# Performance work log

Measured on AMD Instinct MI355X. Metric: run time of the kernel, lower is better.

Reference implementation:

```python
import jax, jax.numpy as jnp
import numpy as np

EMB = 256
D_INNER = 512                         # expand=2 * d_model
HEADDIM = 64
NHEADS = D_INNER // HEADDIM           # 8
DSTATE = 128
DCONV = 4
CONV_DIM = D_INNER + 2 * DSTATE       # 768 (ngroups=1)
D_IN_PROJ = 2 * D_INNER + 2 * DSTATE + NHEADS  # 1288
LN_EPS = 1e-5


def _layernorm(x, w, b):
    m = jnp.mean(x, axis=-1, keepdims=True)
    v = jnp.mean((x - m) ** 2, axis=-1, keepdims=True)
    return (x - m) * jax.lax.rsqrt(v + LN_EPS) * w + b


def _wn_linear(x, g, v, b):
    # torch weight_norm(dim=0): w = g * v / ||v|| per output row
    w = g[:, None] * v / jnp.linalg.norm(v, axis=1, keepdims=True)
    return x @ w.T + b


def _ssm_scan(x, dt, A, Bm, Cm):
    # x: (b,l,h,p)  dt: (b,l,h)  A: (h,)  Bm/Cm: (b,l,n)
    dA = jnp.exp(dt * A)           # (b,l,h), A<0 so dA in (0,1)
    dtx = dt[..., None] * x        # (b,l,h,p)
    bsz = x.shape[0]

    def step(h, inp):
        dA_t, dtx_t, B_t, C_t = inp
        h = h * dA_t[:, :, None, None] + dtx_t[..., None] * B_t[:, None, None, :]
        y = jnp.einsum('bhpn,bn->bhp', h, C_t)
        return h, y

    h0 = jnp.zeros((bsz, NHEADS, HEADDIM, DSTATE), x.dtype)
    xs = (jnp.swapaxes(dA, 0, 1), jnp.swapaxes(dtx, 0, 1),
          jnp.swapaxes(Bm, 0, 1), jnp.swapaxes(Cm, 0, 1))
    _, ys = jax.lax.scan(step, h0, xs)
    return jnp.swapaxes(ys, 0, 1)  # (b,l,h,p)


def _mamba2(u, in_proj_w, conv_w, conv_b, dt_bias, A_log, D_param, ssm_norm_w, out_proj_w):
    B, L, _ = u.shape
    zxbcdt = u @ in_proj_w.T                       # (B,L,1288)
    z_gate = zxbcdt[..., :D_INNER]
    xBC = zxbcdt[..., D_INNER:D_INNER + CONV_DIM]
    dt = zxbcdt[..., D_INNER + CONV_DIM:]
    # causal depthwise conv1d
    xp = jnp.pad(xBC, ((0, 0), (DCONV - 1, 0), (0, 0)))
    xc = jax.lax.conv_general_dilated(
        jnp.swapaxes(xp, 1, 2), conv_w[:, None, :], (1,), 'VALID',
        feature_group_count=CONV_DIM, dimension_numbers=('NCH', 'OIH', 'NCH'))
    xc = jax.nn.silu(jnp.swapaxes(xc, 1, 2) + conv_b)
    x = xc[..., :D_INNER].reshape(B, L, NHEADS, HEADDIM)
    Bm = xc[..., D_INNER:D_INNER + DSTATE]
    Cm = xc[..., D_INNER + DSTATE:]
    dt = jax.nn.softplus(dt + dt_bias)             # (B,L,H)
    A = -jnp.exp(A_log)                            # (H,)
    y = _ssm_scan(x, dt, A, Bm, Cm) + D_param[None, None, :, None] * x
    y = y.reshape(B, L, D_INNER)
    # gated RMSNorm (norm_before_gate=False): rmsnorm(y * silu(z)) * w
    yg = y * jax.nn.silu(z_gate)
    yn = yg * jax.lax.rsqrt(jnp.mean(yg ** 2, axis=-1, keepdims=True) + LN_EPS) * ssm_norm_w
    return yn @ out_proj_w.T


def setup_inputs() -> dict:
    key = jax.random.key(0)
    ks = jax.random.split(key, 12)
    B, NU, NA = 1, 64, 512

    def rn(k, shape, scale):
        return jax.random.normal(k, shape, dtype=jnp.float32) * scale

    z = rn(ks[0], (B, NU, NA, EMB), 1.0)
    in_proj_w = rn(ks[1], (D_IN_PROJ, EMB), EMB ** -0.5)
    conv_w = rn(ks[2], (CONV_DIM, DCONV), DCONV ** -0.5)
    conv_b = rn(ks[3], (CONV_DIM,), 0.02)
    dt_bias = jnp.log(jnp.expm1(jax.random.uniform(ks[4], (NHEADS,), minval=0.001, maxval=0.1)))
    A_log = jnp.log(jax.random.uniform(ks[5], (NHEADS,), minval=1.0, maxval=16.0))
    D_param = jnp.ones((NHEADS,), dtype=jnp.float32)
    ssm_norm_w = jnp.ones((D_INNER,), dtype=jnp.float32)
    out_proj_w = rn(ks[6], (EMB, D_INNER), D_INNER ** -0.5)
    ff_v = rn(ks[7], (EMB, EMB), EMB ** -0.5)
    ff_g = jnp.linalg.norm(ff_v, axis=1)
    ff_b = jnp.zeros((EMB,), dtype=jnp.float32)
    fc1_v = rn(ks[8], (EMB, EMB), EMB ** -0.5)
    fc1_g = jnp.linalg.norm(fc1_v, axis=1)
    fc1_b = jnp.zeros((EMB,), dtype=jnp.float32)
    fc2_v = rn(ks[9], (EMB, EMB), EMB ** -0.5)
    fc2_g = jnp.linalg.norm(fc2_v, axis=1)
    fc2_b = jnp.zeros((EMB,), dtype=jnp.float32)
    return {
        'z': z,
        'ln1_w': jnp.ones((EMB,), dtype=jnp.float32), 'ln1_b': jnp.zeros((EMB,), dtype=jnp.float32),
        'in_proj_w': in_proj_w, 'conv_w': conv_w, 'conv_b': conv_b,
        'dt_bias': dt_bias, 'A_log': A_log, 'D_param': D_param,
        'ssm_norm_w': ssm_norm_w, 'out_proj_w': out_proj_w,
        'ff_g': ff_g, 'ff_v': ff_v, 'ff_b': ff_b,
        'ln2_w': jnp.ones((EMB,), dtype=jnp.float32), 'ln2_b': jnp.zeros((EMB,), dtype=jnp.float32),
        'fc1_g': fc1_g, 'fc1_v': fc1_v, 'fc1_b': fc1_b,
        'fc2_g': fc2_g, 'fc2_v': fc2_v, 'fc2_b': fc2_b,
    }


def reference(z, ln1_w, ln1_b, in_proj_w, conv_w, conv_b, dt_bias, A_log, D_param,
              ssm_norm_w, out_proj_w, ff_g, ff_v, ff_b, ln2_w, ln2_b,
              fc1_g, fc1_v, fc1_b, fc2_g, fc2_v, fc2_b):
    b, nu, na, e = z.shape
    # MambaBlock: z + ff(mamba(norm(z)))
    u = _layernorm(z, ln1_w, ln1_b).reshape(-1, na, e)
    y = _mamba2(u, in_proj_w, conv_w, conv_b, dt_bias, A_log, D_param, ssm_norm_w, out_proj_w)
    y = _wn_linear(y, ff_g, ff_v, ff_b).reshape(b, nu, na, e)
    z = z + y
    # NormFF: z + Lin2(GELU(Lin1(LN(z))))  (dropout inactive in eval)
    h = _layernorm(z, ln2_w, ln2_b)
    h = jax.nn.gelu(_wn_linear(h, fc1_g, fc1_v, fc1_b), approximate=False)
    h = _wn_linear(h, fc2_g, fc2_v, fc2_b)
    return z + h
```

## Files before the change

### kernel.cpp

```cpp
#include <hip/hip_runtime.h>
#include <stdint.h>
#include <math.h>

#define EMB       256
#define D_INNER   512
#define HEADDIM   64
#define NHEADS    8
#define DSTATE    128
#define DCONV     4
#define CONV_DIM  768
#define LN_EPS    1e-5f
#define NBATCH    64
#define SEQLEN    512
#define NTOK      (NBATCH*SEQLEN)

typedef __attribute__((ext_vector_type(8))) short          short8;
typedef __attribute__((ext_vector_type(8))) unsigned short u16x8;
typedef __attribute__((ext_vector_type(4))) unsigned short u16x4;
typedef __attribute__((ext_vector_type(4))) float          f32x4;

__device__ __forceinline__ float bfb(unsigned short u) {
    union { unsigned int i; float f; } x; x.i = ((unsigned int)u) << 16; return x.f;
}
__device__ __forceinline__ unsigned short fbf(float f) {
    union { float f; unsigned int i; } x; x.f = f;
    unsigned int i = x.i;
    unsigned int lsb = (i >> 16) & 1u;
    i += 0x7fffu + lsb;
    return (unsigned short)(i >> 16);
}

__device__ __forceinline__ void gld16(const unsigned short* g, unsigned short* l) {
    __builtin_amdgcn_global_load_lds((const __attribute__((address_space(1))) void*)g,
                                     (__attribute__((address_space(3))) void*)l, 16, 0, 0);
}

__global__ __launch_bounds__(256) void cvt2_k(const float* __restrict__ a, unsigned short* __restrict__ oa, int na,
                                              const float* __restrict__ b, unsigned short* __restrict__ ob, int nb) {
    int i = blockIdx.x * 256 + threadIdx.x;
    if (i < na) oa[i] = fbf(a[i]);
    else { i -= na; if (i < nb) ob[i] = fbf(b[i]); }
}

__global__ __launch_bounds__(256) void wnorm3_k(const float* __restrict__ g0, const float* __restrict__ v0, unsigned short* __restrict__ o0,
                                                const float* __restrict__ g1, const float* __restrict__ v1, unsigned short* __restrict__ o1,
                                                const float* __restrict__ g2, const float* __restrict__ v2, unsigned short* __restrict__ o2) {
    int o = blockIdx.x & 255, s = blockIdx.x >> 8, tid = threadIdx.x;
    const float* g = s == 0 ? g0 : (s == 1 ? g1 : g2);
    const float* v = s == 0 ? v0 : (s == 1 ? v1 : v2);
    unsigned short* wout = s == 0 ? o0 : (s == 1 ? o1 : o2);
    float x = v[(size_t)o * 256 + tid];
    float q = x * x;
    __shared__ float sm[4];
    #pragma unroll
    for (int d = 32; d; d >>= 1) q += __shfl_down(q, d);
    if ((tid & 63) == 0) sm[tid >> 6] = q;
    __syncthreads();
    float tot = sm[0] + sm[1] + sm[2] + sm[3];
    float scale = g[o] * rsqrtf(tot);
    wout[(size_t)o * 256 + tid] = fbf(x * scale);
}

__global__ __launch_bounds__(256) void wco_k(const unsigned short* __restrict__ wff,
                                             const unsigned short* __restrict__ outWb,
                                             unsigned short* __restrict__ wco) {
    int i = blockIdx.x, tid = threadIdx.x;
    __shared__ float row[256];
    row[tid] = bfb(wff[(size_t)i * 256 + tid]);
    __syncthreads();
    #pragma unroll
    for (int half = 0; half < 2; half++) {
        int k = tid + half * 256;
        float acc = 0.f;
        for (int j = 0; j < 256; j++)
            acc += row[j] * bfb(outWb[(size_t)j * 512 + k]);
        wco[(size_t)i * 512 + k] = fbf(acc);
    }
}

__global__ __launch_bounds__(256) void ln_k(const float* __restrict__ in,
                                            const float* __restrict__ w,
                                            const float* __restrict__ b,
                                            unsigned short* __restrict__ out) {
    int tok = blockIdx.x, tid = threadIdx.x;
    size_t idx = (size_t)tok * 256 + tid;
    float x = in[idx];
    __shared__ float sm[8];
    float s = x;
    #pragma unroll
    for (int o = 32; o; o >>= 1) s += __shfl_down(s, o);
    if ((tid & 63) == 0) sm[tid >> 6] = s;
    __syncthreads();
    float mean = (sm[0] + sm[1] + sm[2] + sm[3]) * (1.f / 256.f);
    float d = x - mean;
    float q = d * d;
    #pragma unroll
    for (int o = 32; o; o >>= 1) q += __shfl_down(q, o);
    if ((tid & 63) == 0) sm[4 + (tid >> 6)] = q;
    __syncthreads();
    float var = (sm[4] + sm[5] + sm[6] + sm[7]) * (1.f / 256.f);
    out[idx] = fbf(d * rsqrtf(var + LN_EPS) * w[tid] + b[tid]);
}

#define BMT 128
#define BNT 128
#define BKT 32
template<int EPI, int NBN>
__global__ __launch_bounds__(256, 2) void gemm_k(const unsigned short* __restrict__ A,
                                                 const unsigned short* __restrict__ Bw,
                                                 int K, int N,
                                                 unsigned short* __restrict__ out_b,
                                                 float* __restrict__ out_f,
                                                 const float* __restrict__ bias,
                                                 const float* __restrict__ res_f,
                                                 unsigned short* __restrict__ out2_b) {
    __shared__ __align__(16) unsigned short smem[16384];
    int tid = threadIdx.x;
    int d = blockIdx.x;
    const int cpx = (256 * NBN) >> 3;
    int logical = (d & 7) * cpx + (d >> 3);
    int bm = logical / NBN;
    int bn = logical % NBN;
    int lane = tid & 63, w = tid >> 6;
    int wr = w >> 1, wc = w & 1;
    int fr = lane & 15, fq = lane >> 4;

    int rsub = w * 16 + (lane >> 2);
    int cl   = ((lane & 3) ^ ((rsub >> 1) & 3)) << 3;
    const unsigned short* gA0 = A  + (size_t)(bm * BMT + rsub)      * K + cl;
    const unsigned short* gA1 = A  + (size_t)(bm * BMT + rsub + 64) * K + cl;
    const unsigned short* gB0 = Bw + (size_t)(bn * BNT + rsub)      * K + cl;
    const unsigned short* gB1 = Bw + (size_t)(bn * BNT + rsub + 64) * K + cl;

    f32x4 acc[4][4];
    #pragma unroll
    for (int m = 0; m < 4; m++)
        #pragma unroll
        for (int n = 0; n < 4; n++)
            #pragma unroll
            for (int r = 0; r < 4; r++) acc[m][n][r] = 0.f;

    auto AS = [&](int buf) { return &smem[buf * 4096]; };
    auto BS = [&](int buf) { return &smem[8192 + buf * 4096]; };
    auto STAGE = [&](int buf, int k0) {
        gld16(gA0 + k0, AS(buf) + w * 512);
        gld16(gA1 + k0, AS(buf) + 2048 + w * 512);
        gld16(gB0 + k0, BS(buf) + w * 512);
        gld16(gB1 + k0, BS(buf) + 2048 + w * 512);
    };

    int nt = K / BKT;
    STAGE(0, 0);
    STAGE(1, BKT);
    for (int t = 0; t < nt; ++t) {
        int buf = t & 1;
        if (t < nt - 1) asm volatile("s_waitcnt vmcnt(4)" ::: "memory");
        else            asm volatile("s_waitcnt vmcnt(0)" ::: "memory");
        __builtin_amdgcn_s_barrier();
        short8 af[4], bf_[4];
        #pragma unroll
        for (int m = 0; m < 4; m++) {
            int ra = wr * 64 + m * 16 + fr;
            af[m] = *(const short8*)&AS(buf)[ra * 32 + ((fq ^ ((ra >> 1) & 3)) << 3)];
        }
        #pragma unroll
        for (int n = 0; n < 4; n++) {
            int rb = wc * 64 + n * 16 + fr;
            bf_[n] = *(const short8*)&BS(buf)[rb * 32 + ((fq ^ ((rb >> 1) & 3)) << 3)];
        }
        asm volatile("s_waitcnt lgkmcnt(0)" ::: "memory");
        __builtin_amdgcn_sched_barrier(0);
        __builtin_amdgcn_s_barrier();
        if (t + 2 < nt) STAGE(buf, (t + 2) * BKT);
        __builtin_amdgcn_s_setprio(1);
        #pragma unroll
        for (int m = 0; m < 4; m++)
            #pragma unroll
            for (int n = 0; n < 4; n++)
                acc[m][n] = __builtin_amdgcn_mfma_f32_16x16x32_bf16(af[m], bf_[n], acc[m][n], 0, 0, 0);
        __builtin_amdgcn_s_setprio(0);
    }
    __builtin_amdgcn_s_barrier();

    if (EPI == 1 && bn == 10) {
        #pragma unroll
        for (int m = 0; m < 4; m++)
            #pragma unroll
            for (int n = 0; n < 4; n++)
                #pragma unroll
                for (int r = 0; r < 4; r++) {
                    int grow = bm * BMT + wr * 64 + m * 16 + fq * 4 + r;
                    int gcol = 1280 + wc * 64 + n * 16 + fr;
                    if (gcol < 1288) {
                        float a2 = acc[m][n][r] + bias[gcol - 1280];
                        out_f[(size_t)grow * 8 + (gcol - 1280)] =
                            a2 > 20.f ? a2 : log1pf(expf(a2));
                    }
                }
    } else if (EPI == 0 || EPI == 1) {
        unsigned short* cb = smem;
        #pragma unroll
        for (int s = 0; s < 2; s++) {
            if (wr == s) {
                #pragma unroll
                for (int m = 0; m < 4; m++)
                    #pragma unroll
                    for (int n = 0; n < 4; n++)
                        #pragma unroll
                        for (int r = 0; r < 4; r++)
                            cb[(m * 16 + fq * 4 + r) * 136 + wc * 64 + n * 16 + fr] =
                                fbf(acc[m][n][r]);
            }
            __syncthreads();
            #pragma unroll
            for (int k = 0; k < 4; k++) {
                int g = k * 256 + tid;
                int row = g >> 4, col = (g & 15) << 3;
                u16x8 v = *(const u16x8*)&cb[row * 136 + col];
                int grow = bm * BMT + s * 64 + row;
                int gc = bn * BNT + col;
                if (EPI == 0) {
                    *(u16x8*)&out_b[(size_t)grow * N + gc] = v;
                } else {
                    if (gc < 512) *(u16x8*)&out_b[(size_t)grow * 512 + gc] = v;
                    else          *(u16x8*)&out2_b[(size_t)grow * 768 + (gc - 512)] = v;
                }
            }
            __syncthreads();
        }
    } else {
        float* fb = (float*)smem;
        #pragma unroll
        for (int s = 0; s < 4; s++) {
            if (wr == (s >> 1)) {
                int mp = s & 1;
                #pragma unroll
                for (int mm = 0; mm < 2; mm++)
                    #pragma unroll
                    for (int n = 0; n < 4; n++)
                        #pragma unroll
                        for (int r = 0; r < 4; r++)
                            fb[(mm * 16 + fq * 4 + r) * 132 + wc * 64 + n * 16 + fr] =
                                acc[mp * 2 + mm][n][r];
            }
            __syncthreads();
            #pragma unroll
            for (int k = 0; k < 4; k++) {
                int g = k * 256 + tid;
                int row = g >> 5, col = (g & 31) << 2;
                f32x4 v = *(const f32x4*)&fb[row * 132 + col];
                int grow = bm * BMT + (s >> 1) * 64 + (s & 1) * 32 + row;
                int gc = bn * BNT + col;
                size_t idx = (size_t)grow * 256 + gc;
                if (EPI == 2) {
                    f32x4 rr = *(const f32x4*)&res_f[idx];
                    f32x4 o;
                    #pragma unroll
                    for (int j = 0; j < 4; j++) o[j] = rr[j] + v[j] + bias[gc + j];
                    *(f32x4*)&out_f[idx] = o;
                } else {
                    u16x4 o;
                    #pragma unroll
                    for (int j = 0; j < 4; j++) {
                        float x = v[j] + bias[gc + j];
                        o[j] = fbf(0.5f * x * (1.f + erff(x * 0.70710678118654752f)));
                    }
                    *(u16x4*)&out_b[idx] = o;
                }
            }
            __syncthreads();
        }
    }
}

__global__ __launch_bounds__(256) void halo_k(const unsigned short* __restrict__ xbc,
                                              unsigned short* __restrict__ halo) {
    int blk = blockIdx.x;
    int b = blk / 3, c = blk % 3 + 1;
    int tid = threadIdx.x;
    for (int i = tid; i < 288; i += 256) {
        int j = i / 96, off = (i % 96) * 8;
        size_t tok = (size_t)b * 512 + c * 128 - 3 + j;
        *(u16x8*)&halo[((size_t)(b * 4 + c) * 3 + j) * 768 + off] =
            *(const u16x8*)&xbc[tok * 768 + off];
    }
}

__global__ __launch_bounds__(256) void conv_k(unsigned short* xbc,
                                              const unsigned short* __restrict__ halo,
                                              const float* __restrict__ cw,
                                              const float* __restrict__ cb) {
    int b  = blockIdx.y;
    int c  = blockIdx.z;
    int c0 = blockIdx.x * 64;
    int t0 = c * 128;
    int tid = threadIdx.x;
    int cth = tid & 63;
    int rq  = tid >> 6;
    __shared__ unsigned short sraw[131][72];

    int ca = c0 + cth;
    float w0 = cw[ca * 4 + 0], w1 = cw[ca * 4 + 1];
    float w2 = cw[ca * 4 + 2], w3 = cw[ca * 4 + 3];
    float bias = cb[ca];

    if (tid < 192) {
        int j = tid >> 6, cc = tid & 63;
        sraw[j][cc] = (c == 0) ? (unsigned short)0
            : halo[((size_t)(b * 4 + c) * 3 + j) * 768 + c0 + cc];
    }
    for (int idx = tid; idx < 1024; idx += 256) {
        int lt = idx >> 3, cg = idx & 7;
        *(u16x8*)&sraw[3 + lt][cg * 8] =
            *(const u16x8*)&xbc[((size_t)(b * 512 + t0 + lt)) * 768 + c0 + cg * 8];
    }
    __syncthreads();
    #pragma unroll 4
    for (int i = 0; i < 32; i++) {
        int lt = rq + 4 * i;
        float acc = bias
            + bfb(sraw[lt + 0][cth]) * w0
            + bfb(sraw[lt + 1][cth]) * w1
            + bfb(sraw[lt + 2][cth]) * w2
            + bfb(sraw[lt + 3][cth]) * w3;
        acc = acc / (1.f + expf(-acc));
        xbc[((size_t)(b * 512 + t0 + lt)) * 768 + c0 + cth] = fbf(acc);
    }
}

#define CPAD 136
#define TPAD 56
#define TOFF(r) ((((r) >> 4) & 3) << 3)
__global__ __launch_bounds__(256) void ssd_k(const unsigned short* __restrict__ xc,
                                             const float* __restrict__ dts,
                                             const float* __restrict__ A_log,
                                             const float* __restrict__ D_param,
                                             unsigned short* __restrict__ y) {
    __shared__ unsigned short Ct[32][CPAD];
    __shared__ unsigned short Bt[32][CPAD];
    __shared__ unsigned short BtT[128][TPAD];
    __shared__ unsigned short DXT[64][TPAD];
    __shared__ unsigned short LG[32][40];
    __shared__ unsigned short hB[64][CPAD];
    __shared__ unsigned short Yb[32][72];
    __shared__ float scum[32], sdt2[32], sEC[32];
    __shared__ float sET[32][36];

    int d = blockIdx.x;
    int b = (d & 7) | (((d >> 6) & 7) << 3);
    int h = (d >> 3) & 7;
    int tid = threadIdx.x;
    int w = tid >> 6;
    int lane = tid & 63;
    int fr = lane & 15, fq = lane >> 4;

    float A_h = -expf(A_log[h]);
    float D_h = D_param[h];

    f32x4 hacc[8];
    #pragma unroll
    for (int nf = 0; nf < 8; nf++)
        #pragma unroll
        for (int r = 0; r < 4; r++) hacc[nf][r] = 0.f;

    int t  = tid >> 3;
    int e8 = tid & 7;

    u16x8 bv0, bv1, cv0, cv1, xv;
    {
        const unsigned short* row = &xc[((size_t)b * 512 + t) * 768];
        bv0 = *(const u16x8*)&row[512 + e8 * 16];
        bv1 = *(const u16x8*)&row[512 + e8 * 16 + 8];
        cv0 = *(const u16x8*)&row[640 + e8 * 16];
        cv1 = *(const u16x8*)&row[640 + e8 * 16 + 8];
        xv  = *(const u16x8*)&row[h * 64 + e8 * 8];
    }

    for (int c = 0; c < 16; ++c) {
        size_t tok0 = (size_t)b * 512 + c * 32;
        *(u16x8*)&Ct[t][e8 * 16]     = cv0;
        *(u16x8*)&Ct[t][e8 * 16 + 8] = cv1;
        *(u16x8*)&Bt[t][e8 * 16]     = bv0;
        *(u16x8*)&Bt[t][e8 * 16 + 8] = bv1;
        if (tid < 32) {
            float dtv = dts[(tok0 + tid) * 8 + h];
            sdt2[tid] = dtv;
            float la = dtv * A_h;
            #pragma unroll
            for (int dd = 1; dd < 32; dd <<= 1) {
                float up = __shfl_up(la, dd);
                if (lane >= dd) la += up;
            }
            scum[tid] = la;
        }
        __syncthreads();
        float cumQ = scum[31];
        if (tid < 32) sEC[tid] = expf(scum[tid]);
        {
            float dtv = sdt2[t];
            float wgt = expf(cumQ - scum[t]);
            int tof = TOFF(e8 * 16);
            #pragma unroll
            for (int j = 0; j < 8; j++) {
                float dtx = dtv * bfb(xv[j]);
                int rr = e8 * 8 + j;
                DXT[rr][t + TOFF(rr)] = fbf(dtx);
                BtT[e8 * 16 + j][t + tof]     = fbf(wgt * bfb(bv0[j]));
                BtT[e8 * 16 + 8 + j][t + tof] = fbf(wgt * bfb(bv1[j]));
            }
        }
        #pragma unroll
        for (int k = 0; k < 4; k++) {
            int idx = tid * 4 + k;
            int tt = idx >> 5, tq = idx & 31;
            sET[tt][tq] = (tq <= tt) ? expf(scum[tt] - scum[tq]) : 0.f;
        }
        #pragma unroll
        for (int nf = 0; nf < 8; nf++)
            #pragma unroll
            for (int r = 0; r < 4; r++)
                hB[w * 16 + fq * 4 + r][nf * 16 + fr] = fbf(hacc[nf][r]);
        u16x8 nbv0, nbv1, ncv0, ncv1, nxv;
        {
            size_t ptok = (c + 1 < 16) ? (tok0 + 32 + t) : (tok0 + t);
            const unsigned short* row = &xc[ptok * 768];
            nbv0 = *(const u16x8*)&row[512 + e8 * 16];
            nbv1 = *(const u16x8*)&row[512 + e8 * 16 + 8];
            ncv0 = *(const u16x8*)&row[640 + e8 * 16];
            ncv1 = *(const u16x8*)&row[640 + e8 * 16 + 8];
            nxv  = *(const u16x8*)&row[h * 64 + e8 * 8];
        }
        __syncthreads();
        {
            int m = w >> 1, nf = w & 1;
            f32x4 g;
            #pragma unroll
            for (int r = 0; r < 4; r++) g[r] = 0.f;
            #pragma unroll
            for (int ks = 0; ks < 4; ks++) {
                short8 ca = *(const short8*)&Ct[m * 16 + fr][ks * 32 + fq * 8];
                short8 bb = *(const short8*)&Bt[nf * 16 + fr][ks * 32 + fq * 8];
                g = __builtin_amdgcn_mfma_f32_16x16x32_bf16(ca, bb, g, 0, 0, 0);
            }
            #pragma unroll
            for (int r = 0; r < 4; r++) {
                int tt = m * 16 + fq * 4 + r;
                int tq = nf * 16 + fr;
                LG[tt][tq] = fbf(g[r] * sET[tt][tq]);
            }
        }
        __syncthreads();
        f32x4 Yi[2];
        #pragma unroll
        for (int m = 0; m < 2; m++)
            #pragma unroll
            for (int r = 0; r < 4; r++) Yi[m][r] = 0.f;
        #pragma unroll
        for (int ks = 0; ks < 4; ks++) {
            short8 a0 = *(const short8*)&Ct[fr][ks * 32 + fq * 8];
            short8 a1 = *(const short8*)&Ct[16 + fr][ks * 32 + fq * 8];
            short8 hb = *(const short8*)&hB[w * 16 + fr][ks * 32 + fq * 8];
            Yi[0] = __builtin_amdgcn_mfma_f32_16x16x32_bf16(a0, hb, Yi[0], 0, 0, 0);
            Yi[1] = __builtin_amdgcn_mfma_f32_16x16x32_bf16(a1, hb, Yi[1], 0, 0, 0);
        }
        #pragma unroll
        for (int m = 0; m < 2; m++)
            #pragma unroll
            for (int r = 0; r < 4; r++) Yi[m][r] *= sEC[m * 16 + fq * 4 + r];
        {
            int wof = TOFF(w * 16);
            short8 a0 = *(const short8*)&LG[fr][fq * 8];
            short8 a1 = *(const short8*)&LG[16 + fr][fq * 8];
            short8 dx = *(const short8*)&DXT[w * 16 + fr][fq * 8 + wof];
            Yi[0] = __builtin_amdgcn_mfma_f32_16x16x32_bf16(a0, dx, Yi[0], 0, 0, 0);
            Yi[1] = __builtin_amdgcn_mfma_f32_16x16x32_bf16(a1, dx, Yi[1], 0, 0, 0);
        }
        {
            float ecq = sEC[31];
            #pragma unroll
            for (int nf = 0; nf < 8; nf++)
                #pragma unroll
                for (int r = 0; r < 4; r++) hacc[nf][r] *= ecq;
            int wof = TOFF(w * 16);
            short8 ax = *(const short8*)&DXT[w * 16 + fr][fq * 8 + wof];
            #pragma unroll
            for (int nf = 0; nf < 8; nf++) {
                short8 bb = *(const short8*)&BtT[nf * 16 + fr][fq * 8 + TOFF(nf * 16)];
                hacc[nf] = __builtin_amdgcn_mfma_f32_16x16x32_bf16(ax, bb, hacc[nf], 0, 0, 0);
            }
        }
        #pragma unroll
        for (int m = 0; m < 2; m++)
            #pragma unroll
            for (int r = 0; r < 4; r++) {
                int tt = m * 16 + fq * 4 + r;
                Yb[tt][w * 16 + fr] = fbf(Yi[m][r]);
            }
        __syncthreads();
        {
            u16x8 yv = *(const u16x8*)&Yb[t][e8 * 8];
            u16x8 ov;
            #pragma unroll
            for (int j = 0; j < 8; j++)
                ov[j] = fbf(bfb(yv[j]) + D_h * bfb(xv[j]));
            *(u16x8*)&y[(tok0 + t) * 512 + h * 64 + e8 * 8] = ov;
        }
        bv0 = nbv0; bv1 = nbv1; cv0 = ncv0; cv1 = ncv1; xv = nxv;
    }
}

__global__ __launch_bounds__(256) void gate_k(const unsigned short* __restrict__ y,
                                              const unsigned short* __restrict__ zg,
                                              const float* __restrict__ nw,
                                              unsigned short* __restrict__ yn) {
    int tok = blockIdx.x, tid = threadIdx.x;
    size_t base = (size_t)tok * 512;
    float gv[2];
    float q = 0.f;
    #pragma unroll
    for (int j = 0; j < 2; j++) {
        int c = tid + j * 256;
        float yy = bfb(y[base + c]);
        float zz = bfb(zg[base + c]);
        float s = zz / (1.f + expf(-zz));
        float t = yy * s;
        gv[j] = t;
        q += t * t;
    }
    __shared__ float sm[4];
    #pragma unroll
    for (int o = 32; o; o >>= 1) q += __shfl_down(q, o);
    if ((tid & 63) == 0) sm[tid >> 6] = q;
    __syncthreads();
    float ms = (sm[0] + sm[1] + sm[2] + sm[3]) * (1.f / 512.f);
    float r = rsqrtf(ms + LN_EPS);
    #pragma unroll
    for (int j = 0; j < 2; j++) {
        int c = tid + j * 256;
        yn[base + c] = fbf(gv[j] * r * nw[c]);
    }
}

extern "C" void kernel_launch(void* const* d_in, const int* in_sizes, int n_in,
                              void* d_out, int out_size, void* d_ws, size_t ws_size,
                              hipStream_t stream) {
    if (n_in < 22) return;
    static const int setup_sizes[22] = {8388608,256,256,329728,3072,768,8,8,8,512,
                                        131072,256,65536,256,256,256,256,65536,256,256,65536,256};
    for (int i = 0; i < 22; i++) if (in_sizes[i] != setup_sizes[i]) return;

    const float* z      = (const float*)d_in[0];
    const float* ln1w   = (const float*)d_in[1];
    const float* ln1b   = (const float*)d_in[2];
    const float* inW    = (const float*)d_in[3];
    const float* convw  = (const float*)d_in[4];
    const float* convb  = (const float*)d_in[5];
    const float* dtb    = (const float*)d_in[6];
    const float* Alog   = (const float*)d_in[7];
    const float* Dp     = (const float*)d_in[8];
    const float* normw  = (const float*)d_in[9];
    const float* outW   = (const float*)d_in[10];
    const float* ffg    = (const float*)d_in[11];
    const float* ffv    = (const float*)d_in[12];
    const float* ffb    = (const float*)d_in[13];
    const float* ln2w   = (const float*)d_in[14];
    const float* ln2b   = (const float*)d_in[15];
    const float* fc1g   = (const float*)d_in[16];
    const float* fc1v   = (const float*)d_in[17];
    const float* fc1b   = (const float*)d_in[18];
    const float* fc2g   = (const float*)d_in[19];
    const float* fc2v   = (const float*)d_in[20];
    const float* fc2b   = (const float*)d_in[21];
    float* out = (float*)d_out;
    (void)out_size;

    char* ws = (char*)d_ws;
    const size_t SLOT_A = (size_t)NTOK * 768 * 2;
    const size_t SLOT_B = (size_t)NTOK * 512 * 2;
    const size_t SLOT_C = (size_t)NTOK * 512 * 2;
    const size_t SLOT_D = (size_t)NTOK * 256 * 2;
    const size_t SLOT_E = (size_t)NTOK * 8 * 4;
    const size_t SLOT_W = (size_t)256 * 256 * 2;
    const size_t SLOT_WI = (size_t)1288 * 256 * 2;
    const size_t SLOT_WO = (size_t)256 * 512 * 2;
    const size_t SLOT_WC = (size_t)256 * 512 * 2;
    const size_t SLOT_H  = (size_t)256 * 3 * 768 * 2;
    char* pA = ws;
    char* pB = pA + SLOT_A;
    char* pC = pB + SLOT_B;
    char* pD = pC + SLOT_C;
    char* pE = pD + SLOT_D;
    char* pW = pE + SLOT_E;
    char* pWI = pW + 3 * SLOT_W;
    char* pWO = pWI + SLOT_WI;
    char* pWC = pWO + SLOT_WO;
    char* pH  = pWC + SLOT_WC;
    size_t need = SLOT_A + SLOT_B + SLOT_C + SLOT_D + SLOT_E + 3 * SLOT_W + SLOT_WI + SLOT_WO + SLOT_WC + SLOT_H;
    if (ws_size < need) return;

    unsigned short* xbc = (unsigned short*)pA;
    unsigned short* yn  = (unsigned short*)pA;
    unsigned short* t2  = (unsigned short*)(pA + (size_t)NTOK * 512 * 2);
    unsigned short* y   = (unsigned short*)pB;
    float*          z2  = (float*)pB;
    unsigned short* zgb = (unsigned short*)pC;
    unsigned short* u   = (unsigned short*)pD;
    unsigned short* h1  = (unsigned short*)pD;
    float*          dts = (float*)pE;
    unsigned short* wff  = (unsigned short*)pW;
    unsigned short* wfc1 = (unsigned short*)(pW + SLOT_W);
    unsigned short* wfc2 = (unsigned short*)(pW + 2 * SLOT_W);
    unsigned short* inWb = (unsigned short*)pWI;
    unsigned short* outWb = (unsigned short*)pWO;
    unsigned short* wco  = (unsigned short*)pWC;
    unsigned short* halo = (unsigned short*)pH;

    cvt2_k<<<(1288 * 256 + 131072 + 255) / 256, 256, 0, stream>>>(inW, inWb, 1288 * 256,
                                                                  outW, outWb, 131072);
    wnorm3_k<<<768, 256, 0, stream>>>(ffg, ffv, wff, fc1g, fc1v, wfc1, fc2g, fc2v, wfc2);
    wco_k<<<256, 256, 0, stream>>>(wff, outWb, wco);
    ln_k<<<NTOK, 256, 0, stream>>>(z, ln1w, ln1b, u);
    gemm_k<1, 11><<<256 * 11, 256, 0, stream>>>(u, inWb, 256, 1288,
                                                zgb, dts, dtb, nullptr, xbc);
    halo_k<<<192, 256, 0, stream>>>(xbc, halo);
    conv_k<<<dim3(12, 64, 4), 256, 0, stream>>>(xbc, halo, convw, convb);
    ssd_k<<<NBATCH * NHEADS, 256, 0, stream>>>(xbc, dts, Alog, Dp, y);
    gate_k<<<NTOK, 256, 0, stream>>>(y, zgb, normw, yn);
    gemm_k<2, 2><<<256 * 2, 256, 0, stream>>>(yn, wco, 512, 256,
                                              nullptr, z2, ffb, z, nullptr);
    ln_k<<<NTOK, 256, 0, stream>>>(z2, ln2w, ln2b, t2);
    gemm_k<3, 2><<<256 * 2, 256, 0, stream>>>(t2, wfc1, 256, 256,
                                              h1, nullptr, fc1b, nullptr, nullptr);
    gemm_k<2, 2><<<256 * 2, 256, 0, stream>>>(h1, wfc2, 256, 256,
                                              nullptr, out, fc2b, z2, nullptr);
}
```

Before: 290.2 us.

## Split SSD scan over state dimension halves to double block count

Adds an ssd2_k kernel that splits the 128-wide state dimension into two halves of 64, launching 1024 blocks instead of 512 so more of the GPU is occupied during the sequential chunk scan. Each half writes a partial output to a separate buffer, and gate_k sums the two partials before gating. The extra buffer is used only when the workspace is large enough, otherwise the old path runs. The cost is redundant recomputation of the intra-chunk terms and dt cumsums in both halves, an extra 32 MB output write and read, and partial sums rounded to bf16 before they are added.

```diff
diff --git a/kernel.cpp b/kernel.cpp
--- a/kernel.cpp
+++ b/kernel.cpp
@@ -331,6 +331,7 @@
 #define CPAD 136
 #define TPAD 56
 #define TOFF(r) ((((r) >> 4) & 3) << 3)
+
 __global__ __launch_bounds__(256) void ssd_k(const unsigned short* __restrict__ xc,
                                              const float* __restrict__ dts,
                                              const float* __restrict__ A_log,
@@ -509,7 +510,187 @@
     }
 }
 
+#define CPAD2 72
+__global__ __launch_bounds__(256) void ssd2_k(const unsigned short* __restrict__ xc,
+                                              const float* __restrict__ dts,
+                                              const float* __restrict__ A_log,
+                                              const float* __restrict__ D_param,
+                                              unsigned short* __restrict__ y0,
+                                              unsigned short* __restrict__ y1) {
+    __shared__ unsigned short Ct[32][CPAD2];
+    __shared__ unsigned short Bt[32][CPAD2];
+    __shared__ unsigned short BtT[64][TPAD];
+    __shared__ unsigned short DXT[64][TPAD];
+    __shared__ unsigned short LG[32][40];
+    __shared__ unsigned short hB[64][CPAD2];
+    __shared__ unsigned short Yb[32][72];
+    __shared__ float scum[32], sdt2[32], sEC[32];
+    __shared__ float sET[32][36];
+
+    int d = blockIdx.x;
+    int b  = (d & 7) | (((d >> 7) & 7) << 3);
+    int h  = (d >> 3) & 7;
+    int ph = (d >> 6) & 1;
+    int n0 = ph << 6;
+    unsigned short* yo = ph ? y1 : y0;
+    int tid = threadIdx.x;
+    int w = tid >> 6;
+    int lane = tid & 63;
+    int fr = lane & 15, fq = lane >> 4;
+
+    float A_h = -expf(A_log[h]);
+    float D_h = D_param[h];
+
+    f32x4 hacc[4];
+    #pragma unroll
+    for (int nf = 0; nf < 4; nf++)
+        #pragma unroll
+        for (int r = 0; r < 4; r++) hacc[nf][r] = 0.f;
+
+    int t  = tid >> 3;
+    int e8 = tid & 7;
+
+    u16x8 bv, cv, xv;
+    {
+        const unsigned short* row = &xc[((size_t)b * 512 + t) * 768];
+        bv = *(const u16x8*)&row[512 + n0 + e8 * 8];
+        cv = *(const u16x8*)&row[640 + n0 + e8 * 8];
+        xv = *(const u16x8*)&row[h * 64 + e8 * 8];
+    }
+
+    for (int c = 0; c < 16; ++c) {
+        size_t tok0 = (size_t)b * 512 + c * 32;
+        *(u16x8*)&Ct[t][e8 * 8] = cv;
+        *(u16x8*)&Bt[t][e8 * 8] = bv;
+        if (tid < 32) {
+            float dtv = dts[(tok0 + tid) * 8 + h];
+            sdt2[tid] = dtv;
+            float la = dtv * A_h;
+            #pragma unroll
+            for (int dd = 1; dd < 32; dd <<= 1) {
+                float up = __shfl_up(la, dd);
+                if (lane >= dd) la += up;
+            }
+            scum[tid] = la;
+        }
+        __syncthreads();
+        float cumQ = scum[31];
+        if (tid < 32) sEC[tid] = expf(scum[tid]);
+        {
+            float dtv = sdt2[t];
+            float wgt = expf(cumQ - scum[t]);
+            #pragma unroll
+            for (int j = 0; j < 8; j++) {
+                int rr = e8 * 8 + j;
+                DXT[rr][t + TOFF(rr)] = fbf(dtv * bfb(xv[j]));
+                BtT[rr][t + TOFF(rr)] = fbf(wgt * bfb(bv[j]));
+            }
+        }
+        #pragma unroll
+        for (int k = 0; k < 4; k++) {
+            int idx = tid * 4 + k;
+            int tt = idx >> 5, tq = idx & 31;
+            sET[tt][tq] = (tq <= tt) ? expf(scum[tt] - scum[tq]) : 0.f;
+        }
+        #pragma unroll
+        for (int nf = 0; nf < 4; nf++)
+            #pragma unroll
+            for (int r = 0; r < 4; r++)
+                hB[w * 16 + fq * 4 + r][nf * 16 + fr] = fbf(hacc[nf][r]);
+        u16x8 nbv, ncv, nxv;
+        {
+            size_t ptok = (c + 1 < 16) ? (tok0 + 32 + t) : (tok0 + t);
+            const unsigned short* row = &xc[ptok * 768];
+            nbv = *(const u16x8*)&row[512 + n0 + e8 * 8];
+            ncv = *(const u16x8*)&row[640 + n0 + e8 * 8];
+            nxv = *(const u16x8*)&row[h * 64 + e8 * 8];
+        }
+        __syncthreads();
+        {
+            int m = w >> 1, nf = w & 1;
+            f32x4 g;
+            #pragma unroll
+            for (int r = 0; r < 4; r++) g[r] = 0.f;
+            #pragma unroll
+            for (int ks = 0; ks < 2; ks++) {
+                short8 ca = *(const short8*)&Ct[m * 16 + fr][ks * 32 + fq * 8];
+                short8 bb = *(const short8*)&Bt[nf * 16 + fr][ks * 32 + fq * 8];
+                g = __builtin_amdgcn_mfma_f32_16x16x32_bf16(ca, bb, g, 0, 0, 0);
+            }
+            #pragma unroll
+            for (int r = 0; r < 4; r++) {
+                int tt = m * 16 + fq * 4 + r;
+                int tq = nf * 16 + fr;
+                LG[tt][tq] = fbf(g[r] * sET[tt][tq]);
+            }
+        }
+        __syncthreads();
+        f32x4 Yi[2];
+        #pragma unroll
+        for (int m = 0; m < 2; m++)
+            #pragma unroll
+            for (int r = 0; r < 4; r++) Yi[m][r] = 0.f;
+        #pragma unroll
+        for (int ks = 0; ks < 2; ks++) {
+            short8 a0 = *(const short8*)&Ct[fr][ks * 32 + fq * 8];
+            short8 a1 = *(const short8*)&Ct[16 + fr][ks * 32 + fq * 8];
+            short8 hb = *(const short8*)&hB[w * 16 + fr][ks * 32 + fq * 8];
+            Yi[0] = __builtin_amdgcn_mfma_f32_16x16x32_bf16(a0, hb, Yi[0], 0, 0, 0);
+            Yi[1] = __builtin_amdgcn_mfma_f32_16x16x32_bf16(a1, hb, Yi[1], 0, 0, 0);
+        }
+        #pragma unroll
+        for (int m = 0; m < 2; m++)
+            #pragma unroll
+            for (int r = 0; r < 4; r++) Yi[m][r] *= sEC[m * 16 + fq * 4 + r];
+        {
+            int wof = TOFF(w * 16);
+            short8 a0 = *(const short8*)&LG[fr][fq * 8];
+            short8 a1 = *(const short8*)&LG[16 + fr][fq * 8];
+            short8 dx = *(const short8*)&DXT[w * 16 + fr][fq * 8 + wof];
+            Yi[0] = __builtin_amdgcn_mfma_f32_16x16x32_bf16(a0, dx, Yi[0], 0, 0, 0);
+            Yi[1] = __builtin_amdgcn_mfma_f32_16x16x32_bf16(a1, dx, Yi[1], 0, 0, 0);
+        }
+        {
+            float ecq = sEC[31];
+            #pragma unroll
+            for (int nf = 0; nf < 4; nf++)
+                #pragma unroll
+                for (int r = 0; r < 4; r++) hacc[nf][r] *= ecq;
+            int wof = TOFF(w * 16);
+            short8 ax = *(const short8*)&DXT[w * 16 + fr][fq * 8 + wof];
+            #pragma unroll
+            for (int nf = 0; nf < 4; nf++) {
+                short8 bb = *(const short8*)&BtT[nf * 16 + fr][fq * 8 + TOFF(nf * 16)];
+                hacc[nf] = __builtin_amdgcn_mfma_f32_16x16x32_bf16(ax, bb, hacc[nf], 0, 0, 0);
+            }
+        }
+        #pragma unroll
+        for (int m = 0; m < 2; m++)
+            #pragma unroll
+            for (int r = 0; r < 4; r++) {
+                int tt = m * 16 + fq * 4 + r;
+                Yb[tt][w * 16 + fr] = fbf(Yi[m][r]);
+            }
+        __syncthreads();
+        {
+            u16x8 yv = *(const u16x8*)&Yb[t][e8 * 8];
+            u16x8 ov;
+            if (ph == 0) {
+                #pragma unroll
+                for (int j = 0; j < 8; j++)
+                    ov[j] = fbf(bfb(yv[j]) + D_h * bfb(xv[j]));
+            } else {
+                ov = yv;
+            }
+            *(u16x8*)&yo[(tok0 + t) * 512 + h * 64 + e8 * 8] = ov;
+        }
+        bv = nbv; cv = ncv; xv = nxv;
+    }
+}
+
+template<int TWO>
 __global__ __launch_bounds__(256) void gate_k(const unsigned short* __restrict__ y,
+                                              const unsigned short* __restrict__ y1,
                                               const unsigned short* __restrict__ zg,
                                               const float* __restrict__ nw,
                                               unsigned short* __restrict__ yn) {
@@ -521,6 +702,7 @@
     for (int j = 0; j < 2; j++) {
         int c = tid + j * 256;
         float yy = bfb(y[base + c]);
+        if (TWO) yy += bfb(y1[base + c]);
         float zz = bfb(zg[base + c]);
         float s = zz / (1.f + expf(-zz));
         float t = yy * s;
@@ -585,6 +767,7 @@
     const size_t SLOT_WO = (size_t)256 * 512 * 2;
     const size_t SLOT_WC = (size_t)256 * 512 * 2;
     const size_t SLOT_H  = (size_t)256 * 3 * 768 * 2;
+    const size_t SLOT_Y2 = (size_t)NTOK * 512 * 2;
     char* pA = ws;
     char* pB = pA + SLOT_A;
     char* pC = pB + SLOT_B;
@@ -595,8 +778,10 @@
     char* pWO = pWI + SLOT_WI;
     char* pWC = pWO + SLOT_WO;
     char* pH  = pWC + SLOT_WC;
+    char* pY2 = pH + SLOT_H;
     size_t need = SLOT_A + SLOT_B + SLOT_C + SLOT_D + SLOT_E + 3 * SLOT_W + SLOT_WI + SLOT_WO + SLOT_WC + SLOT_H;
     if (ws_size < need) return;
+    bool split = (ws_size >= need + SLOT_Y2);
 
     unsigned short* xbc = (unsigned short*)pA;
     unsigned short* yn  = (unsigned short*)pA;
@@ -614,6 +799,7 @@
     unsigned short* outWb = (unsigned short*)pWO;
     unsigned short* wco  = (unsigned short*)pWC;
     unsigned short* halo = (unsigned short*)pH;
+    unsigned short* y2   = (unsigned short*)pY2;
 
     cvt2_k<<<(1288 * 256 + 131072 + 255) / 256, 256, 0, stream>>>(inW, inWb, 1288 * 256,
                                                                   outW, outWb, 131072);
@@ -624,8 +810,13 @@
                                                 zgb, dts, dtb, nullptr, xbc);
     halo_k<<<192, 256, 0, stream>>>(xbc, halo);
     conv_k<<<dim3(12, 64, 4), 256, 0, stream>>>(xbc, halo, convw, convb);
-    ssd_k<<<NBATCH * NHEADS, 256, 0, stream>>>(xbc, dts, Alog, Dp, y);
-    gate_k<<<NTOK, 256, 0, stream>>>(y, zgb, normw, yn);
+    if (split) {
+        ssd2_k<<<1024, 256, 0, stream>>>(xbc, dts, Alog, Dp, y, y2);
+        gate_k<1><<<NTOK, 256, 0, stream>>>(y, y2, zgb, normw, yn);
+    } else {
+        ssd_k<<<512, 256, 0, stream>>>(xbc, dts, Alog, Dp, y);
+        gate_k<0><<<NTOK, 256, 0, stream>>>(y, nullptr, zgb, normw, yn);
+    }
     gemm_k<2, 2><<<256 * 2, 256, 0, stream>>>(yn, wco, 512, 256,
                                               nullptr, z2, ffb, z, nullptr);
     ln_k<<<NTOK, 256, 0, stream>>>(z2, ln2w, ln2b, t2);
```

Result: slower. 334.6 us (+15.3%).
